# Kernel optimization log

Measured on AMD Instinct MI355X. Metric: run time of the kernel, lower is better.

Reference implementation:

```python
import jax, jax.numpy as jnp
import numpy as np

N_NODES = 50000
N_EDGES = 800000
D = 64
B = 64
HL = 128  # lstm hidden
OUT = 32


def setup_inputs() -> dict:
    key = jax.random.key(0)
    ks = jax.random.split(key, 16)
    s = 0.05
    return {
        "x": jax.random.normal(ks[0], (N_NODES, D), jnp.float32),
        "edge_index": jax.random.randint(ks[1], (2, N_EDGES), 0, N_NODES),
        "batch": jnp.sort(jax.random.randint(ks[2], (N_NODES,), 0, B)),
        "w1": jax.random.normal(ks[3], (D, D), jnp.float32) * s,
        "b1": jnp.zeros((D,), jnp.float32),
        "w2": jax.random.normal(ks[4], (D, D), jnp.float32) * s,
        "b2": jnp.zeros((D,), jnp.float32),
        "w3": jax.random.normal(ks[5], (D, D), jnp.float32) * s,
        "b3": jnp.zeros((D,), jnp.float32),
        "w4": jax.random.normal(ks[6], (D, D), jnp.float32) * s,
        "b4": jnp.zeros((D,), jnp.float32),
        "w_ih": jax.random.normal(ks[7], (4 * HL, D), jnp.float32) * s,
        "w_hh": jax.random.normal(ks[8], (4 * HL, HL), jnp.float32) * s,
        "b_ih": jnp.zeros((4 * HL,), jnp.float32),
        "b_hh": jnp.zeros((4 * HL,), jnp.float32),
        "fc_w": jax.random.normal(ks[9], (OUT, HL), jnp.float32) * s,
        "fc_b": jnp.zeros((OUT,), jnp.float32),
        "h0": jax.random.normal(ks[10], (1, B, HL), jnp.float32),
        "c0": jax.random.normal(ks[11], (1, B, HL), jnp.float32),
    }


def _gin(x, edge_index, wA, bA, wB, bB):
    # GINConv with eps=0: MLP(x + sum_{j->i} x_j); scatter-add over edges
    agg = jax.ops.segment_sum(x[edge_index[0]], edge_index[1], num_segments=N_NODES)
    h = x + agg
    h = jax.nn.relu(h @ wA.T + bA)
    return h @ wB.T + bB


def reference(x, edge_index, batch, w1, b1, w2, b2, w3, b3, w4, b4,
              w_ih, w_hh, b_ih, b_hh, fc_w, fc_b, h0, c0):
    h = jax.nn.relu(_gin(x, edge_index, w1, b1, w2, b2))  # dropout = identity (eval)
    h = jax.nn.relu(_gin(h, edge_index, w3, b3, w4, b4))
    # global_mean_pool over graphs
    sums = jax.ops.segment_sum(h, batch, num_segments=B)              # [B, D]
    cnts = jax.ops.segment_sum(jnp.ones((N_NODES,), h.dtype), batch, num_segments=B)
    pooled = sums / jnp.maximum(cnts, 1.0)[:, None]
    # single-step LSTM (PyTorch gate order: i, f, g, o)
    gates = pooled @ w_ih.T + b_ih + h0[0] @ w_hh.T + b_hh            # [B, 4H]
    i, f, g, o = jnp.split(gates, 4, axis=-1)
    c1 = jax.nn.sigmoid(f) * c0[0] + jax.nn.sigmoid(i) * jnp.tanh(g)
    h1 = jax.nn.sigmoid(o) * jnp.tanh(c1)
    logits = h1 @ fc_w.T + fc_b
    probs = jax.nn.softmax(logits, axis=1)
    return probs, h1[None], c1[None]
```

## Files before the change

kernel.cpp:

```cpp
#include <hip/hip_runtime.h>
#include <hip/hip_bf16.h>

#define N_NODES 50000
#define N_EDGES 800000
#define D 64
#define B 64
#define HL 128
#define OUT 32

#define CAP 64
#define STP 72
#define ZROW N_NODES

#define BINS 196
#define EPB 2048
#define LCAP 48
#define BCAP 4608

#define AB 391
#define CB 3125

typedef __attribute__((ext_vector_type(8))) short          short8;
typedef __attribute__((ext_vector_type(8))) unsigned short ushort8_t;
typedef __attribute__((ext_vector_type(4))) float          floatx4;

__device__ __forceinline__ unsigned short f2bf(float f)
{
    unsigned u = __float_as_uint(f);
    u = (u + 0x7FFFu + ((u >> 16) & 1u)) >> 16;
    return (unsigned short)u;
}
__device__ __forceinline__ float bf2f(unsigned short s)
{
    return __uint_as_float(((unsigned)s) << 16);
}

__global__ __launch_bounds__(256) void fused_pro_kernel(
    const int*   __restrict__ ei,
    int*         __restrict__ bincnt,
    unsigned*    __restrict__ binbuf,
    const float* __restrict__ x, unsigned short* __restrict__ xb,
    const float* __restrict__ w1, const float* __restrict__ w2,
    const float* __restrict__ w3, const float* __restrict__ w4,
    unsigned short* __restrict__ wb,
    unsigned short* __restrict__ h1,
    float*       __restrict__ psum)
{
    __shared__ int      lcnt[BINS];
    __shared__ int      gbase[BINS];
    __shared__ unsigned lbuf[BINS * LCAP];

    int t = threadIdx.x;

    if (blockIdx.x < AB) {
        if (t < BINS) lcnt[t] = 0;
        __syncthreads();

        int base = blockIdx.x * EPB;
#pragma unroll
        for (int i = 0; i < EPB / 256; ++i) {
            int e = base + i * 256 + t;
            if (e < N_EDGES) {
                int s = ei[e];
                int d = ei[N_EDGES + e];
                int bin = d >> 8;
                unsigned pk = (unsigned)s | ((unsigned)(d & 255) << 16);
                int p = atomicAdd(&lcnt[bin], 1);
                if (p < LCAP) {
                    lbuf[bin * LCAP + p] = pk;
                } else {
                    int q = atomicAdd(&bincnt[bin], 1);
                    if (q < BCAP) binbuf[bin * BCAP + q] = pk;
                }
            }
        }
        __syncthreads();

        if (t < BINS) {
            int m = lcnt[t]; m = (m < LCAP) ? m : LCAP;
            gbase[t] = (m > 0) ? atomicAdd(&bincnt[t], m) : 0;
        }
        __syncthreads();

        int wv = t >> 6, lane = t & 63;
        for (int b = wv; b < BINS; b += 4) {
            int m = lcnt[b]; m = (m < LCAP) ? m : LCAP;
            int gb = gbase[b];
            for (int j = lane; j < m; j += 64)
                if (gb + j < BCAP) binbuf[b * BCAP + gb + j] = lbuf[b * LCAP + j];
        }
    } else if (blockIdx.x < AB + CB) {
        int cb = blockIdx.x - AB;
        int i = cb * 256 + t;
        const float4 v = reinterpret_cast<const float4*>(x)[i];
        ushort4 o;
        o.x = f2bf(v.x); o.y = f2bf(v.y); o.z = f2bf(v.z); o.w = f2bf(v.w);
        reinterpret_cast<ushort4*>(xb)[i] = o;

        if (cb < 64) {
            int j = cb * 256 + t;
            int m = j >> 12, off = j & 4095;
            const float* src = (m == 0) ? w1 : (m == 1) ? w2 : (m == 2) ? w3 : w4;
            wb[j] = f2bf(src[off]);
        }
    } else {
        if (t < D) {
            xb[(size_t)ZROW * D + t] = 0;
            h1[(size_t)ZROW * D + t] = 0;
        }
#pragma unroll
        for (int k = 0; k < 16; ++k)
            psum[t * 16 + k] = 0.0f;
    }
}

__global__ __launch_bounds__(256) void binB_kernel(
    const int*      __restrict__ bincnt,
    const unsigned* __restrict__ binbuf,
    int*            __restrict__ cnt,
    unsigned short* __restrict__ bucket)
{
    __shared__ int            lc[256];
    __shared__ unsigned short lbkt[256 * CAP];

    int t = threadIdx.x;
    lc[t] = 0;
    {
        ushort8_t fill = {ZROW, ZROW, ZROW, ZROW, ZROW, ZROW, ZROW, ZROW};
        for (int idx = t; idx < 256 * CAP / 8; idx += 256)
            reinterpret_cast<ushort8_t*>(lbkt)[idx] = fill;
    }
    __syncthreads();

    int bin = blockIdx.x;
    int m = bincnt[bin]; m = (m < BCAP) ? m : BCAP;
    const unsigned* src = binbuf + bin * BCAP;
    for (int j = t; j < m; j += 256) {
        unsigned pk = src[j];
        int dlow = (pk >> 16) & 255;
        int p = atomicAdd(&lc[dlow], 1);
        if (p < CAP) lbkt[dlow * CAP + p] = (unsigned short)(pk & 0xFFFFu);
    }
    __syncthreads();

    int n0 = bin * 256;
    int n = n0 + t;
    if (n < N_NODES) cnt[n] = (lc[t] < CAP) ? lc[t] : CAP;

    for (int idx = t; idx < 256 * 8; idx += 256) {
        int r = idx >> 3, c = idx & 7;
        if (n0 + r < N_NODES)
            *reinterpret_cast<ushort8_t*>(
                bucket + (size_t)(n0 + r) * CAP + c * 8) =
                *reinterpret_cast<const ushort8_t*>(&lbkt[r * CAP + c * 8]);
    }
}

__global__ __launch_bounds__(256) void gather_kernel(
    const unsigned short* __restrict__ feat,
    const int*            __restrict__ cnt,
    const unsigned short* __restrict__ bucket,
    unsigned short*       __restrict__ outp)
{
    int wv = threadIdx.x >> 6, lane = threadIdx.x & 63;
    int n = blockIdx.x * 4 + wv;

    int deg = cnt[n];
    deg = (deg < CAP) ? deg : CAP;
    int rounds = (deg + 15) >> 4;
    const unsigned short* bkt = bucket + (size_t)n * CAP;

    float acc = bf2f(feat[(size_t)n * D + lane]);
    for (int r = 0; r < rounds; ++r) {
        ushort8_t ia = *reinterpret_cast<const ushort8_t*>(bkt + r * 16);
        ushort8_t ib = *reinterpret_cast<const ushort8_t*>(bkt + r * 16 + 8);
        float v0 = bf2f(feat[(size_t)ia[0] * D + lane]);
        float v1 = bf2f(feat[(size_t)ia[1] * D + lane]);
        float v2 = bf2f(feat[(size_t)ia[2] * D + lane]);
        float v3 = bf2f(feat[(size_t)ia[3] * D + lane]);
        float v4 = bf2f(feat[(size_t)ia[4] * D + lane]);
        float v5 = bf2f(feat[(size_t)ia[5] * D + lane]);
        float v6 = bf2f(feat[(size_t)ia[6] * D + lane]);
        float v7 = bf2f(feat[(size_t)ia[7] * D + lane]);
        float v8 = bf2f(feat[(size_t)ib[0] * D + lane]);
        float v9 = bf2f(feat[(size_t)ib[1] * D + lane]);
        float va = bf2f(feat[(size_t)ib[2] * D + lane]);
        float vb = bf2f(feat[(size_t)ib[3] * D + lane]);
        float vc = bf2f(feat[(size_t)ib[4] * D + lane]);
        float vd = bf2f(feat[(size_t)ib[5] * D + lane]);
        float ve = bf2f(feat[(size_t)ib[6] * D + lane]);
        float vf = bf2f(feat[(size_t)ib[7] * D + lane]);
        acc += (((v0 + v1) + (v2 + v3)) + ((v4 + v5) + (v6 + v7)))
             + (((v8 + v9) + (va + vb)) + ((vc + vd) + (ve + vf)));
    }
    outp[(size_t)n * D + lane] = f2bf(acc);
}

__global__ __launch_bounds__(256) void mlp_kernel(
    const unsigned short* __restrict__ feat,
    const unsigned short* __restrict__ wAb,
    const float*          __restrict__ bA,
    const unsigned short* __restrict__ wBb,
    const float*          __restrict__ bB,
    unsigned short*       __restrict__ outp)
{
    __shared__ __align__(16) unsigned short st[4][16 * STP];

    const int wv   = threadIdx.x >> 6;
    const int lane = threadIdx.x & 63;
    const int quad = lane >> 4;
    const int col  = lane & 15;

    const int n0 = (blockIdx.x * 4 + wv) * 16;
    if (n0 >= N_NODES) return;

    float bAl[4], bBl[4];
#pragma unroll
    for (int t = 0; t < 4; ++t) {
        bAl[t] = bA[t * 16 + col];
        bBl[t] = bB[t * 16 + col];
    }

    short8 WA[4][2], WB[4][2];
#pragma unroll
    for (int t = 0; t < 4; ++t)
#pragma unroll
        for (int k = 0; k < 2; ++k) {
            WA[t][k] = *reinterpret_cast<const short8*>(
                wAb + (t * 16 + col) * D + k * 32 + quad * 8);
            WB[t][k] = *reinterpret_cast<const short8*>(
                wBb + (t * 16 + col) * D + k * 32 + quad * 8);
        }

    short8 A0 = *reinterpret_cast<const short8*>(
        feat + (size_t)(n0 + col) * D + 0 * 32 + quad * 8);
    short8 A1 = *reinterpret_cast<const short8*>(
        feat + (size_t)(n0 + col) * D + 1 * 32 + quad * 8);

    unsigned short* stw = &st[wv][0];

#pragma unroll
    for (int t = 0; t < 4; ++t) {
        floatx4 c = {0.0f, 0.0f, 0.0f, 0.0f};
        c = __builtin_amdgcn_mfma_f32_16x16x32_bf16(A0, WA[t][0], c, 0, 0, 0);
        c = __builtin_amdgcn_mfma_f32_16x16x32_bf16(A1, WA[t][1], c, 0, 0, 0);
#pragma unroll
        for (int r = 0; r < 4; ++r) {
            float v = fmaxf(c[r] + bAl[t], 0.0f);
            stw[(quad * 4 + r) * STP + t * 16 + col] = f2bf(v);
        }
    }

    short8 T0 = *reinterpret_cast<const short8*>(stw + col * STP + 0 * 32 + quad * 8);
    short8 T1 = *reinterpret_cast<const short8*>(stw + col * STP + 1 * 32 + quad * 8);

#pragma unroll
    for (int t = 0; t < 4; ++t) {
        floatx4 c = {0.0f, 0.0f, 0.0f, 0.0f};
        c = __builtin_amdgcn_mfma_f32_16x16x32_bf16(T0, WB[t][0], c, 0, 0, 0);
        c = __builtin_amdgcn_mfma_f32_16x16x32_bf16(T1, WB[t][1], c, 0, 0, 0);
#pragma unroll
        for (int r = 0; r < 4; ++r) {
            float v = fmaxf(c[r] + bBl[t], 0.0f);
            outp[(size_t)(n0 + quad * 4 + r) * D + t * 16 + col] = f2bf(v);
        }
    }
}

__global__ __launch_bounds__(256) void mlp2_pool_kernel(
    const unsigned short* __restrict__ feat,
    const unsigned short* __restrict__ wAb,
    const float*          __restrict__ bA,
    const unsigned short* __restrict__ wBb,
    const float*          __restrict__ bB,
    const int*            __restrict__ batch,
    float*                __restrict__ psum)
{
    __shared__ __align__(16) unsigned short st[4][16 * STP];
    __shared__ float pt[64][D + 1];
    __shared__ int   sbatch[64];

    const int tid  = threadIdx.x;
    const int wv   = tid >> 6;
    const int lane = tid & 63;
    const int quad = lane >> 4;
    const int col  = lane & 15;

    const int bn0 = blockIdx.x * 64;
    const int n0  = bn0 + wv * 16;
    const bool active = (n0 < N_NODES);

    if (tid < 64) {
        int n = bn0 + tid;
        sbatch[tid] = (n < N_NODES) ? batch[n] : -1;
    }

    if (active) {
        float bAl[4], bBl[4];
#pragma unroll
        for (int t = 0; t < 4; ++t) {
            bAl[t] = bA[t * 16 + col];
            bBl[t] = bB[t * 16 + col];
        }

        short8 WA[4][2], WB[4][2];
#pragma unroll
        for (int t = 0; t < 4; ++t)
#pragma unroll
            for (int k = 0; k < 2; ++k) {
                WA[t][k] = *reinterpret_cast<const short8*>(
                    wAb + (t * 16 + col) * D + k * 32 + quad * 8);
                WB[t][k] = *reinterpret_cast<const short8*>(
                    wBb + (t * 16 + col) * D + k * 32 + quad * 8);
            }

        short8 A0 = *reinterpret_cast<const short8*>(
            feat + (size_t)(n0 + col) * D + 0 * 32 + quad * 8);
        short8 A1 = *reinterpret_cast<const short8*>(
            feat + (size_t)(n0 + col) * D + 1 * 32 + quad * 8);

        unsigned short* stw = &st[wv][0];

#pragma unroll
        for (int t = 0; t < 4; ++t) {
            floatx4 c = {0.0f, 0.0f, 0.0f, 0.0f};
            c = __builtin_amdgcn_mfma_f32_16x16x32_bf16(A0, WA[t][0], c, 0, 0, 0);
            c = __builtin_amdgcn_mfma_f32_16x16x32_bf16(A1, WA[t][1], c, 0, 0, 0);
#pragma unroll
            for (int r = 0; r < 4; ++r) {
                float v = fmaxf(c[r] + bAl[t], 0.0f);
                stw[(quad * 4 + r) * STP + t * 16 + col] = f2bf(v);
            }
        }

        short8 T0 = *reinterpret_cast<const short8*>(stw + col * STP + 0 * 32 + quad * 8);
        short8 T1 = *reinterpret_cast<const short8*>(stw + col * STP + 1 * 32 + quad * 8);

#pragma unroll
        for (int t = 0; t < 4; ++t) {
            floatx4 c = {0.0f, 0.0f, 0.0f, 0.0f};
            c = __builtin_amdgcn_mfma_f32_16x16x32_bf16(T0, WB[t][0], c, 0, 0, 0);
            c = __builtin_amdgcn_mfma_f32_16x16x32_bf16(T1, WB[t][1], c, 0, 0, 0);
#pragma unroll
            for (int r = 0; r < 4; ++r) {
                float v = fmaxf(c[r] + bBl[t], 0.0f);
                pt[wv * 16 + quad * 4 + r][t * 16 + col] = v;
            }
        }
    } else {
#pragma unroll
        for (int r = 0; r < 4; ++r)
            pt[wv * 16 + quad * 4 + r][(lane & 15) * 4 + (lane >> 4)] = 0.0f;
        for (int c = 0; c < 4; ++c)
#pragma unroll
            for (int r = 0; r < 4; ++r)
                pt[wv * 16 + quad * 4 + r][c * 16 + col] = 0.0f;
    }
    __syncthreads();

    int q = tid >> 6;
    int d = tid & 63;
    float acc = 0.0f;
    int curg = sbatch[q * 16];
#pragma unroll
    for (int r = 0; r < 16; ++r) {
        int row = q * 16 + r;
        int g = sbatch[row];
        float v = pt[row][d];
        if (g != curg) {
            if (curg >= 0) atomicAdd(&psum[curg * D + d], acc);
            acc = 0.0f;
            curg = g;
        }
        acc += v;
    }
    if (curg >= 0) atomicAdd(&psum[curg * D + d], acc);
}

__device__ __forceinline__ int lower_bound_dev(const int* a, int n, int v)
{
    int lo = 0, hi = n;
    while (lo < hi) {
        int m = (lo + hi) >> 1;
        if (a[m] < v) lo = m + 1; else hi = m;
    }
    return lo;
}

__device__ __forceinline__ float sigmoidf_(float x) { return 1.0f / (1.0f + expf(-x)); }

__global__ __launch_bounds__(512) void head_kernel(
    const float* __restrict__ psum,
    const int*   __restrict__ batch,
    const float* __restrict__ w_ih,
    const float* __restrict__ w_hh,
    const float* __restrict__ b_ih,
    const float* __restrict__ b_hh,
    const float* __restrict__ fc_w,
    const float* __restrict__ fc_b,
    const float* __restrict__ h0,
    const float* __restrict__ c0,
    float*       __restrict__ out_probs,
    float*       __restrict__ out_h1,
    float*       __restrict__ out_c1)
{
    int b = blockIdx.x;
    int j = threadIdx.x;

    __shared__ float sp[D];
    __shared__ float sh[HL];
    __shared__ float gates[4 * HL];
    __shared__ float sh1[HL];
    __shared__ float slog[OUT];

    if (j < D) {
        int start = lower_bound_dev(batch, N_NODES, b);
        int end   = lower_bound_dev(batch, N_NODES, b + 1);
        sp[j] = psum[b * D + j] / fmaxf((float)(end - start), 1.0f);
    } else if (j < D + HL) {
        sh[j - D] = h0[b * HL + (j - D)];
    }
    __syncthreads();

    {
        float acc = b_ih[j] + b_hh[j];
#pragma unroll
        for (int k = 0; k < D; ++k)  acc = fmaf(sp[k], w_ih[j * D + k], acc);
#pragma unroll
        for (int k = 0; k < HL; ++k) acc = fmaf(sh[k], w_hh[j * HL + k], acc);
        gates[j] = acc;
    }
    __syncthreads();

    if (j < HL) {
        float ig = gates[j];
        float fg = gates[HL + j];
        float gg = gates[2 * HL + j];
        float og = gates[3 * HL + j];
        float c  = sigmoidf_(fg) * c0[b * HL + j] + sigmoidf_(ig) * tanhf(gg);
        float hv = sigmoidf_(og) * tanhf(c);
        out_c1[b * HL + j] = c;
        out_h1[b * HL + j] = hv;
        sh1[j] = hv;
    }
    __syncthreads();

    if (j < OUT) {
        float a = fc_b[j];
#pragma unroll
        for (int k = 0; k < HL; ++k) a = fmaf(sh1[k], fc_w[j * HL + k], a);
        slog[j] = a;
    }
    __syncthreads();

    if (j < OUT) {
        float m = -1e30f;
#pragma unroll
        for (int k = 0; k < OUT; ++k) m = fmaxf(m, slog[k]);
        float s = 0.0f;
#pragma unroll
        for (int k = 0; k < OUT; ++k) s += expf(slog[k] - m);
        out_probs[b * OUT + j] = expf(slog[j] - m) / s;
    }
}

extern "C" void kernel_launch(void* const* d_in, const int* in_sizes, int n_in,
                              void* d_out, int out_size, void* d_ws, size_t ws_size,
                              hipStream_t stream)
{
    const float* x     = (const float*)d_in[0];
    const int*   ei    = (const int*)  d_in[1];
    const int*   batch = (const int*)  d_in[2];
    const float* w1    = (const float*)d_in[3];
    const float* b1    = (const float*)d_in[4];
    const float* w2    = (const float*)d_in[5];
    const float* b2    = (const float*)d_in[6];
    const float* w3    = (const float*)d_in[7];
    const float* b3    = (const float*)d_in[8];
    const float* w4    = (const float*)d_in[9];
    const float* b4    = (const float*)d_in[10];
    const float* w_ih  = (const float*)d_in[11];
    const float* w_hh  = (const float*)d_in[12];
    const float* b_ih  = (const float*)d_in[13];
    const float* b_hh  = (const float*)d_in[14];
    const float* fc_w  = (const float*)d_in[15];
    const float* fc_b  = (const float*)d_in[16];
    const float* h0    = (const float*)d_in[17];
    const float* c0    = (const float*)d_in[18];

    const size_t NR = (size_t)N_NODES + 16;
    int* bincnt = (int*)d_ws;
    int* cnt    = bincnt + 256;
    unsigned* binbuf = (unsigned*)(cnt + N_NODES);
    unsigned short* bucket = (unsigned short*)(binbuf + (size_t)BINS * BCAP);
    unsigned short* xb = bucket + (size_t)N_NODES * CAP;
    unsigned short* g  = xb + NR * D;
    unsigned short* h1 = g  + NR * D;
    unsigned short* wb = h1 + NR * D;
    float* psum = (float*)(wb + 4 * D * D);

    float* out_probs = (float*)d_out;
    float* out_h1    = out_probs + B * OUT;
    float* out_c1    = out_h1 + B * HL;

    const int gb = N_NODES / 4;
    const int mb = (N_NODES / 16 + 3) / 4;

    hipMemsetAsync(bincnt, 0, 256 * sizeof(int), stream);
    fused_pro_kernel<<<AB + CB + 1, 256, 0, stream>>>(
        ei, bincnt, binbuf, x, xb, w1, w2, w3, w4, wb, h1, psum);

    binB_kernel<<<BINS, 256, 0, stream>>>(bincnt, binbuf, cnt, bucket);

    gather_kernel<<<gb, 256, 0, stream>>>(xb, cnt, bucket, g);
    mlp_kernel<<<mb, 256, 0, stream>>>(g, wb, b1, wb + 4096, b2, h1);

    gather_kernel<<<gb, 256, 0, stream>>>(h1, cnt, bucket, g);
    mlp2_pool_kernel<<<mb, 256, 0, stream>>>(g, wb + 8192, b3, wb + 12288, b4,
                                             batch, psum);

    head_kernel<<<B, 512, 0, stream>>>(psum, batch, w_ih, w_hh, b_ih, b_hh,
                                       fc_w, fc_b, h0, c0,
                                       out_probs, out_h1, out_c1);
}
```

Before: 209.7 us.

## Fuse neighbor gather into GIN MLP kernels with 16-lane-per-node gathering

Removes the two standalone gather kernels. Each MLP wave now gathers and sums neighbor features for its own 16 nodes directly into its LDS staging tile, which then feeds the MFMA input. This drops the global write and re-read of the aggregated feature buffer and two kernel launches. The gather layout also changes: 16 lanes cover one node with 4-element bf16 vector loads, 4 nodes are processed per wave at once, and the next index chunk is prefetched. The trade-off is far fewer waves doing the latency-bound gather (one launch of MLP-sized blocks), which may hide memory latency less well.

```diff
diff --git a/kernel.cpp b/kernel.cpp
--- a/kernel.cpp
+++ b/kernel.cpp
@@ -34,6 +34,8 @@
 {
     return __uint_as_float(((unsigned)s) << 16);
 }
+__device__ __forceinline__ float bfLO(unsigned u) { return __uint_as_float(u << 16); }
+__device__ __forceinline__ float bfHI(unsigned u) { return __uint_as_float(u & 0xffff0000u); }
 
 __global__ __launch_bounds__(256) void fused_pro_kernel(
     const int*   __restrict__ ei,
@@ -156,48 +158,57 @@
     }
 }
 
-__global__ __launch_bounds__(256) void gather_kernel(
+__device__ __forceinline__ void gather16(
     const unsigned short* __restrict__ feat,
     const int*            __restrict__ cnt,
     const unsigned short* __restrict__ bucket,
-    unsigned short*       __restrict__ outp)
-{
-    int wv = threadIdx.x >> 6, lane = threadIdx.x & 63;
-    int n = blockIdx.x * 4 + wv;
-
-    int deg = cnt[n];
-    deg = (deg < CAP) ? deg : CAP;
-    int rounds = (deg + 15) >> 4;
-    const unsigned short* bkt = bucket + (size_t)n * CAP;
-
-    float acc = bf2f(feat[(size_t)n * D + lane]);
-    for (int r = 0; r < rounds; ++r) {
-        ushort8_t ia = *reinterpret_cast<const ushort8_t*>(bkt + r * 16);
-        ushort8_t ib = *reinterpret_cast<const ushort8_t*>(bkt + r * 16 + 8);
-        float v0 = bf2f(feat[(size_t)ia[0] * D + lane]);
-        float v1 = bf2f(feat[(size_t)ia[1] * D + lane]);
-        float v2 = bf2f(feat[(size_t)ia[2] * D + lane]);
-        float v3 = bf2f(feat[(size_t)ia[3] * D + lane]);
-        float v4 = bf2f(feat[(size_t)ia[4] * D + lane]);
-        float v5 = bf2f(feat[(size_t)ia[5] * D + lane]);
-        float v6 = bf2f(feat[(size_t)ia[6] * D + lane]);
-        float v7 = bf2f(feat[(size_t)ia[7] * D + lane]);
-        float v8 = bf2f(feat[(size_t)ib[0] * D + lane]);
-        float v9 = bf2f(feat[(size_t)ib[1] * D + lane]);
-        float va = bf2f(feat[(size_t)ib[2] * D + lane]);
-        float vb = bf2f(feat[(size_t)ib[3] * D + lane]);
-        float vc = bf2f(feat[(size_t)ib[4] * D + lane]);
-        float vd = bf2f(feat[(size_t)ib[5] * D + lane]);
-        float ve = bf2f(feat[(size_t)ib[6] * D + lane]);
-        float vf = bf2f(feat[(size_t)ib[7] * D + lane]);
-        acc += (((v0 + v1) + (v2 + v3)) + ((v4 + v5) + (v6 + v7)))
-             + (((v8 + v9) + (va + vb)) + ((vc + vd) + (ve + vf)));
-    }
-    outp[(size_t)n * D + lane] = f2bf(acc);
-}
-
-__global__ __launch_bounds__(256) void mlp_kernel(
+    unsigned short*       stw,
+    int n0, int lane)
+{
+    const int g = lane >> 4;
+    const int c = lane & 15;
+
+#pragma unroll
+    for (int b = 0; b < 4; ++b) {
+        const int node = n0 + b * 4 + g;
+        int deg = cnt[node];
+        deg = (deg < CAP) ? deg : CAP;
+        int m = (deg + 7) >> 3;
+        {
+            int t1 = __shfl_xor(m, 16); m = (t1 > m) ? t1 : m;
+            int t2 = __shfl_xor(m, 32); m = (t2 > m) ? t2 : m;
+        }
+
+        const unsigned short* bkt = bucket + (size_t)node * CAP;
+
+        uint2 u = *reinterpret_cast<const uint2*>(feat + (size_t)node * D + 4 * c);
+        float a0 = bfLO(u.x), a1 = bfHI(u.x);
+        float a2 = bfLO(u.y), a3 = bfHI(u.y);
+
+        ushort8_t idx = *reinterpret_cast<const ushort8_t*>(bkt);
+        for (int r = 0; r < m; ++r) {
+            ushort8_t nxt = *reinterpret_cast<const ushort8_t*>(bkt + (r + 1) * 8);
+#pragma unroll
+            for (int j = 0; j < 8; ++j) {
+                uint2 v = *reinterpret_cast<const uint2*>(
+                    feat + (size_t)idx[j] * D + 4 * c);
+                a0 += bfLO(v.x); a1 += bfHI(v.x);
+                a2 += bfLO(v.y); a3 += bfHI(v.y);
+            }
+            idx = nxt;
+        }
+
+        uint2 o;
+        o.x = (unsigned)f2bf(a0) | ((unsigned)f2bf(a1) << 16);
+        o.y = (unsigned)f2bf(a2) | ((unsigned)f2bf(a3) << 16);
+        *reinterpret_cast<uint2*>(stw + (b * 4 + g) * STP + 4 * c) = o;
+    }
+}
+
+__global__ __launch_bounds__(256) void gmlp_kernel(
     const unsigned short* __restrict__ feat,
+    const int*            __restrict__ cnt,
+    const unsigned short* __restrict__ bucket,
     const unsigned short* __restrict__ wAb,
     const float*          __restrict__ bA,
     const unsigned short* __restrict__ wBb,
@@ -232,12 +243,12 @@
                 wBb + (t * 16 + col) * D + k * 32 + quad * 8);
         }
 
-    short8 A0 = *reinterpret_cast<const short8*>(
-        feat + (size_t)(n0 + col) * D + 0 * 32 + quad * 8);
-    short8 A1 = *reinterpret_cast<const short8*>(
-        feat + (size_t)(n0 + col) * D + 1 * 32 + quad * 8);
-
     unsigned short* stw = &st[wv][0];
+
+    gather16(feat, cnt, bucket, stw, n0, lane);
+
+    short8 A0 = *reinterpret_cast<const short8*>(stw + col * STP + 0 * 32 + quad * 8);
+    short8 A1 = *reinterpret_cast<const short8*>(stw + col * STP + 1 * 32 + quad * 8);
 
 #pragma unroll
     for (int t = 0; t < 4; ++t) {
@@ -267,8 +278,10 @@
     }
 }
 
-__global__ __launch_bounds__(256) void mlp2_pool_kernel(
+__global__ __launch_bounds__(256) void g2mlp_pool_kernel(
     const unsigned short* __restrict__ feat,
+    const int*            __restrict__ cnt,
+    const unsigned short* __restrict__ bucket,
     const unsigned short* __restrict__ wAb,
     const float*          __restrict__ bA,
     const unsigned short* __restrict__ wBb,
@@ -314,12 +327,12 @@
                     wBb + (t * 16 + col) * D + k * 32 + quad * 8);
             }
 
-        short8 A0 = *reinterpret_cast<const short8*>(
-            feat + (size_t)(n0 + col) * D + 0 * 32 + quad * 8);
-        short8 A1 = *reinterpret_cast<const short8*>(
-            feat + (size_t)(n0 + col) * D + 1 * 32 + quad * 8);
-
         unsigned short* stw = &st[wv][0];
+
+        gather16(feat, cnt, bucket, stw, n0, lane);
+
+        short8 A0 = *reinterpret_cast<const short8*>(stw + col * STP + 0 * 32 + quad * 8);
+        short8 A1 = *reinterpret_cast<const short8*>(stw + col * STP + 1 * 32 + quad * 8);
 
 #pragma unroll
         for (int t = 0; t < 4; ++t) {
@@ -498,12 +511,12 @@
     unsigned short* h1 = g  + NR * D;
     unsigned short* wb = h1 + NR * D;
     float* psum = (float*)(wb + 4 * D * D);
+    (void)g;
 
     float* out_probs = (float*)d_out;
     float* out_h1    = out_probs + B * OUT;
     float* out_c1    = out_h1 + B * HL;
 
-    const int gb = N_NODES / 4;
     const int mb = (N_NODES / 16 + 3) / 4;
 
     hipMemsetAsync(bincnt, 0, 256 * sizeof(int), stream);
@@ -512,12 +525,11 @@
 
     binB_kernel<<<BINS, 256, 0, stream>>>(bincnt, binbuf, cnt, bucket);
 
-    gather_kernel<<<gb, 256, 0, stream>>>(xb, cnt, bucket, g);
-    mlp_kernel<<<mb, 256, 0, stream>>>(g, wb, b1, wb + 4096, b2, h1);
-
-    gather_kernel<<<gb, 256, 0, stream>>>(h1, cnt, bucket, g);
-    mlp2_pool_kernel<<<mb, 256, 0, stream>>>(g, wb + 8192, b3, wb + 12288, b4,
-                                             batch, psum);
+    gmlp_kernel<<<mb, 256, 0, stream>>>(xb, cnt, bucket, wb, b1, wb + 4096, b2, h1);
+
+    g2mlp_pool_kernel<<<mb, 256, 0, stream>>>(h1, cnt, bucket,
+                                              wb + 8192, b3, wb + 12288, b4,
+                                              batch, psum);
 
     head_kernel<<<B, 512, 0, stream>>>(psum, batch, w_ih, w_hh, b_ih, b_hh,
                                        fc_w, fc_b, h0, c0,
```

Result: faster. 202.2 us (-3.6%).
